# Performance work log

Measured on AMD Instinct MI355X. Metric: run time of the kernel, lower is better.

The kernel has to match this reference:

```python
import jax, jax.numpy as jnp
import numpy as np


def psf2otf(psf, shape):
    """Zero-pad psf to `shape` and circularly shift so its center is at the
    origin, then 2D FFT. psf: [..., kh, kw] -> complex [..., H, W]."""
    kh, kw = psf.shape[-2], psf.shape[-1]
    H, W = shape
    pad = jnp.zeros(psf.shape[:-2] + (H, W), psf.dtype)
    pad = pad.at[..., :kh, :kw].set(psf)
    pad = jnp.roll(pad, shift=(-(kh // 2), -(kw // 2)), axis=(-2, -1))
    return jnp.fft.fft2(pad)


def setup_inputs() -> dict:
    key = jax.random.key(0)
    k1, k2, k3, k4, k5 = jax.random.split(key, 5)
    B, C, H, W = 4, 3, 512, 512
    NF, FS, KS = 24, 5, 25
    y = jax.random.normal(k1, (B, C, H, W), dtype=jnp.float32)
    k = jax.random.uniform(k2, (B, 1, KS, KS), dtype=jnp.float32)
    k = k / jnp.sum(k, axis=(-2, -1), keepdims=True)  # normalized blur PSF
    w = 0.5 + jax.random.uniform(k3, (B, 1), dtype=jnp.float32)  # positive (Softplus output)
    phi = jax.random.normal(k4, (B, C, H, W), dtype=jnp.float32)
    weights = jax.random.normal(k5, (NF, C, FS, FS), dtype=jnp.float32) * 0.3
    return {"y": y, "k": k, "w": w, "phi": phi, "weights": weights}


def reference(y, k, w, phi, weights):
    # FFT-domain Wiener deconvolution (FourierDeconvolutionFunction_init.forward).
    B, C, H, W = y.shape
    Fy = jnp.fft.fft2(y)                         # [B,C,H,W] complex64
    Dg = psf2otf(weights, (H, W))                # [NF,C,H,W] complex64
    Dk = psf2otf(k, (H, W))                      # [B,1,H,W] complex64, broadcasts over C
    w4 = w[:, :, None, None]                     # [B,1,1,1]
    Fphi = jnp.fft.fft2(phi / w4)                # [B,C,H,W]
    Dg_sum = jnp.sum(jnp.abs(Dg) ** 2, axis=0)[None] / w4   # [B,C,H,W] real
    Omega = 1.0 / (jnp.abs(Dk) ** 2 + Dg_sum)    # [B,C,H,W] real
    num = Omega * (jnp.conj(Dk) * Fy + Fphi)     # [B,C,H,W] complex64
    out = jnp.real(jnp.fft.ifft2(num)).astype(y.dtype)  # torch.irfft(..., onesided=False)
    return out
```

## Files before the change

kernel.cpp:

```cpp
#include <hip/hip_runtime.h>
#include <math.h>

#define PI_F 3.14159265358979323846f
#define NPIX 262144

__device__ __forceinline__ float2 cmul(float2 a, float2 b) {
    return make_float2(a.x * b.x - a.y * b.y, a.x * b.y + a.y * b.x);
}
__device__ __forceinline__ float2 cadd(float2 a, float2 b) {
    return make_float2(a.x + b.x, a.y + b.y);
}
__device__ __forceinline__ float2 csub(float2 a, float2 b) {
    return make_float2(a.x - b.x, a.y - b.y);
}

template<int DIR>
__device__ __forceinline__ void fill_tw(float2* tw, int t, int stride) {
    for (int m = t; m < 384; m += stride) {
        const float ang = (2.0f * PI_F / 512.0f) * (float)m;
        const float s = __sinf(ang), c = __cosf(ang);
        tw[m] = make_float2(c, (DIR > 0) ? s : -s);
    }
}

template<int DIR>
__device__ __forceinline__ float2* fft512(float2* sA, float2* sB,
                                          const float2* tw, int t) {
    float2* X = sA;
    float2* Y = sB;
    int Ns = 1;
#pragma unroll
    for (int s = 0; s < 4; ++s) {
        const int jm = t & (Ns - 1);
        const int jd = t - jm;
        float2 v0 = X[t], v1 = X[t + 128], v2 = X[t + 256], v3 = X[t + 384];
        const int m1 = jm * (128 / Ns);
        v1 = cmul(tw[m1], v1);
        v2 = cmul(tw[2 * m1], v2);
        v3 = cmul(tw[3 * m1], v3);
        const float2 t0 = cadd(v0, v2), t1 = csub(v0, v2);
        const float2 t2 = cadd(v1, v3), t3 = csub(v1, v3);
        const float2 t3i = (DIR > 0) ? make_float2(-t3.y, t3.x)
                                     : make_float2(t3.y, -t3.x);
        const int od = (jd << 2) + jm;
        Y[od]          = cadd(t0, t2);
        Y[od + Ns]     = cadd(t1, t3i);
        Y[od + 2 * Ns] = csub(t0, t2);
        Y[od + 3 * Ns] = csub(t1, t3i);
        __syncthreads();
        float2* tmp = X; X = Y; Y = tmp;
        Ns <<= 2;
    }
#pragma unroll
    for (int q = 0; q < 2; ++q) {
        const int j = t + q * 128;
        const float2 a = X[j], b = X[j + 256];
        const float2 tt = cmul(tw[j], b);
        Y[j]       = cadd(a, tt);
        Y[j + 256] = csub(a, tt);
    }
    __syncthreads();
    return Y;
}

__global__ __launch_bounds__(128) void fwd_fft_all(const float* __restrict__ y,
                                                   const float* __restrict__ phi,
                                                   const float* __restrict__ w,
                                                   float2* __restrict__ S) {
    __shared__ float2 sA[512], sB[512], tw[384];
    const int t = threadIdx.x;
    fill_tw<-1>(tw, t, 128);
    if (blockIdx.x < 6144) {
        const int img = blockIdx.x >> 9, row = blockIdx.x & 511;
        const size_t off = (size_t)img * NPIX + (size_t)row * 512;
        const float iwv = 1.0f / w[img / 3];
        const float4 yv = ((const float4*)(y + off))[t];
        const float4 pv = ((const float4*)(phi + off))[t];
        sA[4 * t + 0] = make_float2(yv.x, pv.x * iwv);
        sA[4 * t + 1] = make_float2(yv.y, pv.y * iwv);
        sA[4 * t + 2] = make_float2(yv.z, pv.z * iwv);
        sA[4 * t + 3] = make_float2(yv.w, pv.w * iwv);
        __syncthreads();
        float2* R = fft512<-1>(sA, sB, tw, t);
        float4* wp = (float4*)(S + off);
        for (int k = t; k < 256; k += 128)
            wp[k] = make_float4(R[2 * k].x, R[2 * k].y,
                                R[2 * k + 1].x, R[2 * k + 1].y);
        return;
    }
    const int bid = blockIdx.x - 6144;
    int img, row;
    if (bid < 100) {
        img = 12 + bid / 25;
        row = (bid % 25 - 12) & 511;
    } else {
        const int g = bid - 100;
        img = 16 + g / 9;
        row = ((g % 9) - 4) & 511;
    }
    float2* rp = S + (size_t)img * NPIX + (size_t)row * 512;
    for (int k = t; k < 512; k += 128) sA[k] = rp[k];
    __syncthreads();
    float2* R = fft512<-1>(sA, sB, tw, t);
    for (int k = t; k < 512; k += 128) rp[k] = R[k];
}

template<int DIR>
__global__ __launch_bounds__(128) void fft_rows(float2* __restrict__ D) {
    __shared__ float2 sA[512], sB[512], tw[384];
    const int t = threadIdx.x;
    fill_tw<DIR>(tw, t, 128);
    float2* rp = D + (size_t)blockIdx.x * 512;
    const float4* rp4 = (const float4*)rp;
    for (int k = t; k < 256; k += 128) {
        const float4 v = rp4[k];
        sA[2 * k]     = make_float2(v.x, v.y);
        sA[2 * k + 1] = make_float2(v.z, v.w);
    }
    __syncthreads();
    float2* R = fft512<DIR>(sA, sB, tw, t);
    float4* wp = (float4*)rp;
    for (int k = t; k < 256; k += 128)
        wp[k] = make_float4(R[2 * k].x, R[2 * k].y,
                            R[2 * k + 1].x, R[2 * k + 1].y);
}

__device__ __forceinline__ float2 get2(const float4 a, const float4 b, int q) {
    switch (q) {
        case 0:  return make_float2(a.x, a.y);
        case 1:  return make_float2(a.z, a.w);
        case 2:  return make_float2(b.x, b.y);
        default: return make_float2(b.z, b.w);
    }
}

__global__ __launch_bounds__(256) void combine_ifft(const float2* __restrict__ S,
                                                    const float* __restrict__ w,
                                                    float2* __restrict__ P) {
    __shared__ float2 sA[2][512], sB[2][512], tw[384];
    const int t = threadIdx.x;
    const int h = t >> 7, tt = t & 127;
    const int rr = blockIdx.x;
    const int pair = blockIdx.y;
    const int r0 = rr, r1 = (512 - rr) & 511;
    const int rh = h ? r1 : r0;
    const int ro = h ? r0 : r1;
    fill_tw<1>(tw, t, 256);
    const int i0 = 2 * pair, i1 = 2 * pair + 1;
    const int b0 = i0 / 3, b1 = i1 / 3;
    const int ch0 = i0 % 3, ch1 = i1 % 3;
    const float iw0 = 1.0f / w[b0], iw1 = 1.0f / w[b1];
    const size_t rowh = (size_t)rh * 512, rowo = (size_t)ro * 512;
    const float4* Zv0 = (const float4*)(S + (size_t)i0 * NPIX + rowh);
    const float4* Zv1 = (const float4*)(S + (size_t)i1 * NPIX + rowh);
    const float2* Zn0 = S + (size_t)i0 * NPIX + rowo;
    const float2* Zn1 = S + (size_t)i1 * NPIX + rowo;
    const float4* K0 = (const float4*)(S + (size_t)(12 + b0) * NPIX + rowh);
    const float4* K1 = (const float4*)(S + (size_t)(12 + b1) * NPIX + rowh);
    const float4* G0 = (const float4*)(S + (size_t)(16 + ch0) * NPIX + rowh);
    const float4* G1 = (const float4*)(S + (size_t)(16 + ch1) * NPIX + rowh);

    const float4 za = Zv0[2 * tt], zb = Zv0[2 * tt + 1];
    const float4 ua = Zv1[2 * tt], ub = Zv1[2 * tt + 1];
    const float4 ka = K0[2 * tt],  kb = K0[2 * tt + 1];
    const float4 la = K1[2 * tt],  lb = K1[2 * tt + 1];
    const float4 ga = G0[2 * tt],  gb = G0[2 * tt + 1];
    const float4 ha = G1[2 * tt],  hb = G1[2 * tt + 1];
#pragma unroll
    for (int q = 0; q < 4; ++q) {
        const int c = 4 * tt + q;
        const int nc = (512 - c) & 511;
        float2 num[2];
#pragma unroll
        for (int e = 0; e < 2; ++e) {
            const float2 Zv = e ? get2(ua, ub, q) : get2(za, zb, q);
            const float2 Zn = e ? Zn1[nc] : Zn0[nc];
            const float2 K  = e ? get2(la, lb, q) : get2(ka, kb, q);
            const float dg  = (e ? get2(ha, hb, q).x : get2(ga, gb, q).x) *
                              (e ? iw1 : iw0);
            const float2 Zm = make_float2(Zn.x, -Zn.y);
            const float2 Fy = make_float2(0.5f * (Zv.x + Zm.x),
                                          0.5f * (Zv.y + Zm.y));
            const float dx = Zv.x - Zm.x, dy = Zv.y - Zm.y;
            const float2 Fphi = make_float2(0.5f * dy, -0.5f * dx);
            const float kk = K.x * K.x + K.y * K.y;
            const float Om = 1.0f / (kk + dg);
            const float2 cf = make_float2(K.x * Fy.x + K.y * Fy.y,
                                          K.x * Fy.y - K.y * Fy.x);
            num[e] = make_float2(Om * (cf.x + Fphi.x), Om * (cf.y + Fphi.y));
        }
        sA[h][c] = make_float2(num[0].x - num[1].y, num[0].y + num[1].x);
    }
    __syncthreads();
    float2* R = fft512<1>(&sA[h][0], &sB[h][0], tw, tt);
    if (!(h == 1 && r1 == r0)) {
        float4* wp = (float4*)(P + (size_t)pair * NPIX + rowh);
        for (int k = tt; k < 256; k += 128)
            wp[k] = make_float4(R[2 * k].x, R[2 * k].y,
                                R[2 * k + 1].x, R[2 * k + 1].y);
    }
}

__global__ __launch_bounds__(128) void inv_fft_unpack(const float2* __restrict__ T,
                                                      float* __restrict__ out) {
    __shared__ float2 sA[512], sB[512], tw[384];
    const int t = threadIdx.x;
    const int pair = blockIdx.x >> 9, row = blockIdx.x & 511;
    fill_tw<1>(tw, t, 128);
    const float2* rp = T + (size_t)pair * NPIX + (size_t)row * 512;
    const float4* rp4 = (const float4*)rp;
    for (int k = t; k < 256; k += 128) {
        const float4 v = rp4[k];
        sA[2 * k]     = make_float2(v.x, v.y);
        sA[2 * k + 1] = make_float2(v.z, v.w);
    }
    __syncthreads();
    float2* R = fft512<1>(sA, sB, tw, t);
    const float sc = 1.0f / 262144.0f;
    float* o0 = out + (size_t)(2 * pair) * NPIX + (size_t)row * 512;
    float* o1 = o0 + NPIX;
    ((float4*)o0)[t] = make_float4(R[4 * t].x * sc, R[4 * t + 1].x * sc,
                                   R[4 * t + 2].x * sc, R[4 * t + 3].x * sc);
    ((float4*)o1)[t] = make_float4(R[4 * t].y * sc, R[4 * t + 1].y * sc,
                                   R[4 * t + 2].y * sc, R[4 * t + 3].y * sc);
}

__global__ __launch_bounds__(256) void transpose512_inplace(float2* __restrict__ D) {
    if (blockIdx.x > blockIdx.y) return;
    __shared__ float2 tA[32][33], tB[32][33];
    const size_t base = (size_t)blockIdx.z * NPIX;
    const int bi = blockIdx.x * 32, bj = blockIdx.y * 32;
    const int tx = threadIdx.x, ty = threadIdx.y;
    const bool diag = (bi == bj);
#pragma unroll
    for (int j = 0; j < 32; j += 8)
        tA[ty + j][tx] = D[base + (size_t)(bj + ty + j) * 512 + bi + tx];
    if (!diag) {
#pragma unroll
        for (int j = 0; j < 32; j += 8)
            tB[ty + j][tx] = D[base + (size_t)(bi + ty + j) * 512 + bj + tx];
    }
    __syncthreads();
#pragma unroll
    for (int j = 0; j < 32; j += 8)
        D[base + (size_t)(bi + ty + j) * 512 + bj + tx] = tA[tx][ty + j];
    if (!diag) {
#pragma unroll
        for (int j = 0; j < 32; j += 8)
            D[base + (size_t)(bj + ty + j) * 512 + bi + tx] = tB[tx][ty + j];
    }
}

__global__ __launch_bounds__(256) void transpose512(const float2* __restrict__ in,
                                                    float2* __restrict__ out) {
    __shared__ float2 tile[32][33];
    const size_t base = (size_t)blockIdx.z * NPIX;
    const int bx = blockIdx.x * 32, by = blockIdx.y * 32;
    const int tx = threadIdx.x, ty = threadIdx.y;
#pragma unroll
    for (int j = 0; j < 32; j += 8)
        tile[ty + j][tx] = in[base + (size_t)(by + ty + j) * 512 + bx + tx];
    __syncthreads();
#pragma unroll
    for (int j = 0; j < 32; j += 8)
        out[base + (size_t)(bx + ty + j) * 512 + by + tx] = tile[tx][ty + j];
}

__global__ __launch_bounds__(256) void prep_kg(const float* __restrict__ kin,
                                               const float* __restrict__ wts,
                                               float2* __restrict__ S) {
    const int bid = blockIdx.x, tid = threadIdx.x;
    if (bid < 10) {
        const int t = bid * 256 + tid;
        if (t < 2500) {
            const int b = t / 625, rem = t % 625;
            const int i = rem / 25, j = rem % 25;
            const int r = (i - 12) & 511, c = (j - 12) & 511;
            S[(size_t)(12 + b) * NPIX + (size_t)r * 512 + c] =
                make_float2(kin[t], 0.0f);
        }
        return;
    }
    const int ch = bid - 10;
    __shared__ float gp[24][13][13];
    __shared__ float part[243];
    float* gpf = &gp[0][0][0];
    for (int i = tid; i < 24 * 169; i += 256) gpf[i] = 0.0f;
    __syncthreads();
    for (int i = tid; i < 600; i += 256) {
        const int f = i / 25, rem = i % 25;
        const int x = rem / 5, yy = rem % 5;
        gp[f][x + 4][yy + 4] = wts[(size_t)(f * 3 + ch) * 25 + rem];
    }
    __syncthreads();
    if (tid < 243) {
        const int dpos = tid / 3, seg = tid % 3;
        const int di = dpos / 9 - 4, dj = dpos % 9 - 4;
        float acc = 0.0f;
        for (int f = seg * 8; f < seg * 8 + 8; ++f) {
#pragma unroll
            for (int x = 0; x < 5; ++x)
#pragma unroll
                for (int yy = 0; yy < 5; ++yy)
                    acc += gp[f][x + 4][yy + 4] *
                           gp[f][x + di + 4][yy + dj + 4];
        }
        part[tid] = acc;
    }
    __syncthreads();
    if (tid < 81) {
        const float a = part[tid * 3] + part[tid * 3 + 1] + part[tid * 3 + 2];
        const int di = tid / 9 - 4, dj = tid % 9 - 4;
        const int r = di & 511, c = dj & 511;
        S[(size_t)(16 + ch) * NPIX + (size_t)r * 512 + c] =
            make_float2(a, 0.0f);
    }
}

extern "C" void kernel_launch(void* const* d_in, const int* in_sizes, int n_in,
                              void* d_out, int out_size, void* d_ws, size_t ws_size,
                              hipStream_t stream) {
    const float* y   = (const float*)d_in[0];
    const float* k   = (const float*)d_in[1];
    const float* w   = (const float*)d_in[2];
    const float* phi = (const float*)d_in[3];
    const float* wts = (const float*)d_in[4];
    float* out = (float*)d_out;

    const size_t needed = (size_t)25 * NPIX * sizeof(float2);
    if (ws_size < needed) return;
    float2* S = (float2*)d_ws;
    float2* P = S + (size_t)19 * NPIX;

    hipMemsetAsync(S + (size_t)12 * NPIX, 0,
                   (size_t)7 * NPIX * sizeof(float2), stream);

    prep_kg<<<13, 256, 0, stream>>>(k, wts, S);
    fwd_fft_all<<<6271, 128, 0, stream>>>(y, phi, w, S);

    dim3 tb(32, 8);
    transpose512_inplace<<<dim3(16, 16, 19), tb, 0, stream>>>(S);
    fft_rows<-1><<<19 * 512, 128, 0, stream>>>(S);

    combine_ifft<<<dim3(257, 6), 256, 0, stream>>>(S, w, P);

    transpose512<<<dim3(16, 16, 6), tb, 0, stream>>>(P, S);
    inv_fft_unpack<<<6 * 512, 128, 0, stream>>>(S, out);
}
```

Baseline: 159.4 us.

## Fuse transposes into column FFT kernels that gather 8 columns into shared memory

Removes the separate in-place and out-of-place transpose kernels. The new column-FFT kernels load 8-column strips, transpose them into padded shared memory and run eight 512-point FFTs per 1024-thread block using an in-place single-buffer FFT. Each column's result is written out as a contiguous row, which saves two full global-memory round trips. In exchange, the column reads use only 32-byte segments per row, and the workspace grows to hold a separate output buffer.

```diff
diff --git a/kernel.cpp b/kernel.cpp
--- a/kernel.cpp
+++ b/kernel.cpp
@@ -61,6 +61,43 @@
     }
     __syncthreads();
     return Y;
+}
+
+template<int DIR>
+__device__ __forceinline__ void fft512_1b(float2* X, const float2* tw, int t) {
+    int Ns = 1;
+#pragma unroll
+    for (int s = 0; s < 4; ++s) {
+        const int jm = t & (Ns - 1);
+        const int jd = t - jm;
+        float2 v0 = X[t], v1 = X[t + 128], v2 = X[t + 256], v3 = X[t + 384];
+        __syncthreads();
+        const int m1 = jm * (128 / Ns);
+        v1 = cmul(tw[m1], v1);
+        v2 = cmul(tw[2 * m1], v2);
+        v3 = cmul(tw[3 * m1], v3);
+        const float2 t0 = cadd(v0, v2), t1 = csub(v0, v2);
+        const float2 t2 = cadd(v1, v3), t3 = csub(v1, v3);
+        const float2 t3i = (DIR > 0) ? make_float2(-t3.y, t3.x)
+                                     : make_float2(t3.y, -t3.x);
+        const int od = (jd << 2) + jm;
+        X[od]          = cadd(t0, t2);
+        X[od + Ns]     = cadd(t1, t3i);
+        X[od + 2 * Ns] = csub(t0, t2);
+        X[od + 3 * Ns] = csub(t1, t3i);
+        __syncthreads();
+        Ns <<= 2;
+    }
+    const float2 a0 = X[t],       b0 = X[t + 256];
+    const float2 a1 = X[t + 128], b1 = X[t + 384];
+    __syncthreads();
+    const float2 u0 = cmul(tw[t], b0);
+    const float2 u1 = cmul(tw[t + 128], b1);
+    X[t]       = cadd(a0, u0);
+    X[t + 256] = csub(a0, u0);
+    X[t + 128] = cadd(a1, u1);
+    X[t + 384] = csub(a1, u1);
+    __syncthreads();
 }
 
 __global__ __launch_bounds__(128) void fwd_fft_all(const float* __restrict__ y,
@@ -106,23 +143,28 @@
 }
 
 template<int DIR>
-__global__ __launch_bounds__(128) void fft_rows(float2* __restrict__ D) {
-    __shared__ float2 sA[512], sB[512], tw[384];
+__global__ __launch_bounds__(1024) void col_fft(const float2* __restrict__ in,
+                                                float2* __restrict__ outp) {
+    __shared__ float2 sX[8 * 513], tw[384];
     const int t = threadIdx.x;
-    fill_tw<DIR>(tw, t, 128);
-    float2* rp = D + (size_t)blockIdx.x * 512;
-    const float4* rp4 = (const float4*)rp;
-    for (int k = t; k < 256; k += 128) {
-        const float4 v = rp4[k];
-        sA[2 * k]     = make_float2(v.x, v.y);
-        sA[2 * k + 1] = make_float2(v.z, v.w);
-    }
-    __syncthreads();
-    float2* R = fft512<DIR>(sA, sB, tw, t);
-    float4* wp = (float4*)rp;
-    for (int k = t; k < 256; k += 128)
-        wp[k] = make_float4(R[2 * k].x, R[2 * k].y,
-                            R[2 * k + 1].x, R[2 * k + 1].y);
+    const int img = blockIdx.x >> 6;
+    const int u0 = (blockIdx.x & 63) << 3;
+    fill_tw<DIR>(tw, t, 1024);
+    const float2* ip = in + (size_t)img * NPIX + u0;
+    for (int f = t; f < 2048; f += 1024) {
+        const int row = f >> 2, seg = f & 3;
+        const float4 v = *(const float4*)(ip + (size_t)row * 512 + seg * 2);
+        sX[(seg * 2)     * 513 + row] = make_float2(v.x, v.y);
+        sX[(seg * 2 + 1) * 513 + row] = make_float2(v.z, v.w);
+    }
+    __syncthreads();
+    const int c = t >> 7, tt = t & 127;
+    float2* X = sX + c * 513;
+    fft512_1b<DIR>(X, tw, tt);
+    float4* wp = (float4*)(outp + (size_t)img * NPIX + (size_t)(u0 + c) * 512);
+    for (int k = tt; k < 256; k += 128)
+        wp[k] = make_float4(X[2 * k].x, X[2 * k].y,
+                            X[2 * k + 1].x, X[2 * k + 1].y);
 }
 
 __device__ __forceinline__ float2 get2(const float4 a, const float4 b, int q) {
@@ -134,7 +176,7 @@
     }
 }
 
-__global__ __launch_bounds__(256) void combine_ifft(const float2* __restrict__ S,
+__global__ __launch_bounds__(256) void combine_ifft(const float2* __restrict__ T,
                                                     const float* __restrict__ w,
                                                     float2* __restrict__ P) {
     __shared__ float2 sA[2][512], sB[2][512], tw[384];
@@ -151,14 +193,14 @@
     const int ch0 = i0 % 3, ch1 = i1 % 3;
     const float iw0 = 1.0f / w[b0], iw1 = 1.0f / w[b1];
     const size_t rowh = (size_t)rh * 512, rowo = (size_t)ro * 512;
-    const float4* Zv0 = (const float4*)(S + (size_t)i0 * NPIX + rowh);
-    const float4* Zv1 = (const float4*)(S + (size_t)i1 * NPIX + rowh);
-    const float2* Zn0 = S + (size_t)i0 * NPIX + rowo;
-    const float2* Zn1 = S + (size_t)i1 * NPIX + rowo;
-    const float4* K0 = (const float4*)(S + (size_t)(12 + b0) * NPIX + rowh);
-    const float4* K1 = (const float4*)(S + (size_t)(12 + b1) * NPIX + rowh);
-    const float4* G0 = (const float4*)(S + (size_t)(16 + ch0) * NPIX + rowh);
-    const float4* G1 = (const float4*)(S + (size_t)(16 + ch1) * NPIX + rowh);
+    const float4* Zv0 = (const float4*)(T + (size_t)i0 * NPIX + rowh);
+    const float4* Zv1 = (const float4*)(T + (size_t)i1 * NPIX + rowh);
+    const float2* Zn0 = T + (size_t)i0 * NPIX + rowo;
+    const float2* Zn1 = T + (size_t)i1 * NPIX + rowo;
+    const float4* K0 = (const float4*)(T + (size_t)(12 + b0) * NPIX + rowh);
+    const float4* K1 = (const float4*)(T + (size_t)(12 + b1) * NPIX + rowh);
+    const float4* G0 = (const float4*)(T + (size_t)(16 + ch0) * NPIX + rowh);
+    const float4* G1 = (const float4*)(T + (size_t)(16 + ch1) * NPIX + rowh);
 
     const float4 za = Zv0[2 * tt], zb = Zv0[2 * tt + 1];
     const float4 ua = Zv1[2 * tt], ub = Zv1[2 * tt + 1];
@@ -201,69 +243,31 @@
     }
 }
 
-__global__ __launch_bounds__(128) void inv_fft_unpack(const float2* __restrict__ T,
-                                                      float* __restrict__ out) {
-    __shared__ float2 sA[512], sB[512], tw[384];
+__global__ __launch_bounds__(1024) void col_ifft_unpack(const float2* __restrict__ P,
+                                                        float* __restrict__ out) {
+    __shared__ float2 sX[8 * 513], tw[384];
     const int t = threadIdx.x;
-    const int pair = blockIdx.x >> 9, row = blockIdx.x & 511;
-    fill_tw<1>(tw, t, 128);
-    const float2* rp = T + (size_t)pair * NPIX + (size_t)row * 512;
-    const float4* rp4 = (const float4*)rp;
-    for (int k = t; k < 256; k += 128) {
-        const float4 v = rp4[k];
-        sA[2 * k]     = make_float2(v.x, v.y);
-        sA[2 * k + 1] = make_float2(v.z, v.w);
-    }
-    __syncthreads();
-    float2* R = fft512<1>(sA, sB, tw, t);
+    const int pair = blockIdx.x >> 6;
+    const int s0 = (blockIdx.x & 63) << 3;
+    fill_tw<1>(tw, t, 1024);
+    const float2* ip = P + (size_t)pair * NPIX + s0;
+    for (int f = t; f < 2048; f += 1024) {
+        const int row = f >> 2, seg = f & 3;
+        const float4 v = *(const float4*)(ip + (size_t)row * 512 + seg * 2);
+        sX[(seg * 2)     * 513 + row] = make_float2(v.x, v.y);
+        sX[(seg * 2 + 1) * 513 + row] = make_float2(v.z, v.w);
+    }
+    __syncthreads();
+    const int c = t >> 7, tt = t & 127;
+    float2* X = sX + c * 513;
+    fft512_1b<1>(X, tw, tt);
     const float sc = 1.0f / 262144.0f;
-    float* o0 = out + (size_t)(2 * pair) * NPIX + (size_t)row * 512;
+    float* o0 = out + (size_t)(2 * pair) * NPIX + (size_t)(s0 + c) * 512;
     float* o1 = o0 + NPIX;
-    ((float4*)o0)[t] = make_float4(R[4 * t].x * sc, R[4 * t + 1].x * sc,
-                                   R[4 * t + 2].x * sc, R[4 * t + 3].x * sc);
-    ((float4*)o1)[t] = make_float4(R[4 * t].y * sc, R[4 * t + 1].y * sc,
-                                   R[4 * t + 2].y * sc, R[4 * t + 3].y * sc);
-}
-
-__global__ __launch_bounds__(256) void transpose512_inplace(float2* __restrict__ D) {
-    if (blockIdx.x > blockIdx.y) return;
-    __shared__ float2 tA[32][33], tB[32][33];
-    const size_t base = (size_t)blockIdx.z * NPIX;
-    const int bi = blockIdx.x * 32, bj = blockIdx.y * 32;
-    const int tx = threadIdx.x, ty = threadIdx.y;
-    const bool diag = (bi == bj);
-#pragma unroll
-    for (int j = 0; j < 32; j += 8)
-        tA[ty + j][tx] = D[base + (size_t)(bj + ty + j) * 512 + bi + tx];
-    if (!diag) {
-#pragma unroll
-        for (int j = 0; j < 32; j += 8)
-            tB[ty + j][tx] = D[base + (size_t)(bi + ty + j) * 512 + bj + tx];
-    }
-    __syncthreads();
-#pragma unroll
-    for (int j = 0; j < 32; j += 8)
-        D[base + (size_t)(bi + ty + j) * 512 + bj + tx] = tA[tx][ty + j];
-    if (!diag) {
-#pragma unroll
-        for (int j = 0; j < 32; j += 8)
-            D[base + (size_t)(bj + ty + j) * 512 + bi + tx] = tB[tx][ty + j];
-    }
-}
-
-__global__ __launch_bounds__(256) void transpose512(const float2* __restrict__ in,
-                                                    float2* __restrict__ out) {
-    __shared__ float2 tile[32][33];
-    const size_t base = (size_t)blockIdx.z * NPIX;
-    const int bx = blockIdx.x * 32, by = blockIdx.y * 32;
-    const int tx = threadIdx.x, ty = threadIdx.y;
-#pragma unroll
-    for (int j = 0; j < 32; j += 8)
-        tile[ty + j][tx] = in[base + (size_t)(by + ty + j) * 512 + bx + tx];
-    __syncthreads();
-#pragma unroll
-    for (int j = 0; j < 32; j += 8)
-        out[base + (size_t)(bx + ty + j) * 512 + by + tx] = tile[tx][ty + j];
+    ((float4*)o0)[tt] = make_float4(X[4 * tt].x * sc, X[4 * tt + 1].x * sc,
+                                    X[4 * tt + 2].x * sc, X[4 * tt + 3].x * sc);
+    ((float4*)o1)[tt] = make_float4(X[4 * tt].y * sc, X[4 * tt + 1].y * sc,
+                                    X[4 * tt + 2].y * sc, X[4 * tt + 3].y * sc);
 }
 
 __global__ __launch_bounds__(256) void prep_kg(const float* __restrict__ kin,
@@ -327,10 +331,11 @@
     const float* wts = (const float*)d_in[4];
     float* out = (float*)d_out;
 
-    const size_t needed = (size_t)25 * NPIX * sizeof(float2);
+    const size_t needed = (size_t)38 * NPIX * sizeof(float2);
     if (ws_size < needed) return;
     float2* S = (float2*)d_ws;
-    float2* P = S + (size_t)19 * NPIX;
+    float2* T = S + (size_t)19 * NPIX;
+    float2* P = S;
 
     hipMemsetAsync(S + (size_t)12 * NPIX, 0,
                    (size_t)7 * NPIX * sizeof(float2), stream);
@@ -338,12 +343,9 @@
     prep_kg<<<13, 256, 0, stream>>>(k, wts, S);
     fwd_fft_all<<<6271, 128, 0, stream>>>(y, phi, w, S);
 
-    dim3 tb(32, 8);
-    transpose512_inplace<<<dim3(16, 16, 19), tb, 0, stream>>>(S);
-    fft_rows<-1><<<19 * 512, 128, 0, stream>>>(S);
-
-    combine_ifft<<<dim3(257, 6), 256, 0, stream>>>(S, w, P);
-
-    transpose512<<<dim3(16, 16, 6), tb, 0, stream>>>(P, S);
-    inv_fft_unpack<<<6 * 512, 128, 0, stream>>>(S, out);
-}
+    col_fft<-1><<<19 * 64, 1024, 0, stream>>>(S, T);
+
+    combine_ifft<<<dim3(257, 6), 256, 0, stream>>>(T, w, P);
+
+    col_ifft_unpack<<<6 * 64, 1024, 0, stream>>>(P, out);
+}
```

Result: faster. 148.7 us (-6.7%).
